# Kernel tuning notes

Hardware: AMD Instinct MI355X
Metric: run time of the kernel (lower is better)

The kernel has to match this reference:

```python
import jax, jax.numpy as jnp
import numpy as np

H = 1024
B_DIM = 64  # bottleneck
EPS = 1e-5

def setup_inputs() -> dict:
    key = jax.random.key(0)
    ks = jax.random.split(key, 5)
    x = jax.random.normal(ks[0], (8, 4096, H), dtype=jnp.float32)
    norm_w = jnp.ones((H,), jnp.float32)
    norm_b = jnp.zeros((H,), jnp.float32)
    # nn.Linear default init ~ U(-1/sqrt(fan_in), 1/sqrt(fan_in))
    lim_d = 1.0 / np.sqrt(H)
    down_w = jax.random.uniform(ks[1], (B_DIM, H), jnp.float32, -lim_d, lim_d)
    down_b = jax.random.uniform(ks[2], (B_DIM,), jnp.float32, -lim_d, lim_d)
    # NOTE: original inits up to zeros; we use small random values so the
    # computation (and gradients) are non-degenerate for kernel testing.
    lim_u = 1.0 / np.sqrt(B_DIM)
    up_w = jax.random.uniform(ks[3], (H, B_DIM), jnp.float32, -lim_u, lim_u)
    up_b = jax.random.uniform(ks[4], (H,), jnp.float32, -lim_u, lim_u)
    return {"x": x, "norm_w": norm_w, "norm_b": norm_b,
            "down_w": down_w, "down_b": down_b, "up_w": up_w, "up_b": up_b}

def reference(x, norm_w, norm_b, down_w, down_b, up_w, up_b):
    # LayerNorm over last dim, eps=1e-5 (PyTorch default)
    mu = jnp.mean(x, axis=-1, keepdims=True)
    var = jnp.mean(jnp.square(x - mu), axis=-1, keepdims=True)
    xn = (x - mu) * jax.lax.rsqrt(var + EPS) * norm_w + norm_b
    # down-proj [B,S,H] @ [H,b] -> [B,S,b]
    h = jnp.einsum('bsh,dh->bsd', xn, down_w) + down_b
    h = jax.nn.gelu(h, approximate=False)  # torch nn.GELU default = exact erf
    # up-proj [B,S,b] @ [b,H] -> [B,S,H], residual add
    out = jnp.einsum('bsd,hd->bsh', h, up_w) + up_b
    return x + out
```

## Files before the change

kernel.cpp:

```cpp
#include <hip/hip_runtime.h>


#define HDIM 1024
#define BDIM 64
#define RT   32
#define XPAD 1032
#define GPAD 72

using s16x8 = __attribute__((ext_vector_type(8))) short;
using s16x4 = __attribute__((ext_vector_type(4))) short;
using f32x4 = __attribute__((ext_vector_type(4))) float;
using f32x2 = __attribute__((ext_vector_type(2))) float;

__device__ __forceinline__ short f2bf(float f) {
  unsigned u = __builtin_bit_cast(unsigned, f);
  u += 0x7fffu + ((u >> 16) & 1u);
  return (short)(u >> 16);
}
__device__ __forceinline__ float bf2f(short s) {
  unsigned u = ((unsigned)(unsigned short)s) << 16;
  return __builtin_bit_cast(float, u);
}

extern "C" __global__ void prep_weights(const float* __restrict__ dw,
                                        const float* __restrict__ uw,
                                        short* __restrict__ wsbf) {
  int tid = blockIdx.x * 256 + threadIdx.x;
  const float* src = (tid < 8192) ? dw : uw;
  int off = (tid < 8192) ? tid * 8 : (tid - 8192) * 8;
  f32x4 v0 = *(const f32x4*)(src + off);
  f32x4 v1 = *(const f32x4*)(src + off + 4);
  s16x8 o;
#pragma unroll
  for (int k = 0; k < 4; ++k) { o[k] = f2bf(v0[k]); o[k + 4] = f2bf(v1[k]); }
  *(s16x8*)(wsbf + tid * 8) = o;
}

extern "C" __global__ __launch_bounds__(512, 4)
void adapter_fused(const float* __restrict__ x,
                   const float* __restrict__ nw, const float* __restrict__ nb,
                   const float* __restrict__ db, const float* __restrict__ ub,
                   const short* __restrict__ dwb, const short* __restrict__ uwb,
                   float* __restrict__ out)
{
  __shared__ __align__(16) short xnbf[RT][XPAD];
  __shared__ __align__(16) short gbf[RT][GPAD];
  __shared__ float wln[HDIM];
  __shared__ float bln[HDIM];

  const int t  = threadIdx.x;
  const int rb = blockIdx.x * RT;

  {
    f32x2 w2 = ((const f32x2*)nw)[t];
    f32x2 b2 = ((const f32x2*)nb)[t];
    *(f32x2*)&wln[t * 2] = w2;
    *(f32x2*)&bln[t * 2] = b2;
  }

  const int r  = t >> 4;
  const int cl = t & 15;
  const float* xrow = x + (size_t)(rb + r) * HDIM;
  float sum = 0.f, ssq = 0.f;
#pragma unroll 8
  for (int i = 0; i < 16; ++i) {
    int j4 = i * 16 + cl;
    f32x4 v = ((const f32x4*)xrow)[j4];
    s16x4 s;
#pragma unroll
    for (int k = 0; k < 4; ++k) { float f = v[k]; sum += f; ssq += f * f; s[k] = f2bf(f); }
    *(s16x4*)&xnbf[r][j4 * 4] = s;
  }
#pragma unroll
  for (int m = 1; m < 16; m <<= 1) {
    sum += __shfl_xor(sum, m);
    ssq += __shfl_xor(ssq, m);
  }
  const float mu  = sum * (1.0f / HDIM);
  const float var = ssq * (1.0f / HDIM) - mu * mu;
  const float rs  = rsqrtf(var + 1e-5f);

#pragma unroll
  for (int i = 0; i < 16; ++i) {
    int j = (i * 16 + cl) * 4;
    s16x4 s = *(const s16x4*)&xnbf[r][j];
    s16x4 o;
#pragma unroll
    for (int k = 0; k < 4; ++k) {
      float xf = bf2f(s[k]);
      o[k] = f2bf((xf - mu) * rs * wln[j + k] + bln[j + k]);
    }
    *(s16x4*)&xnbf[r][j] = o;
  }
  __syncthreads();

  const int w    = t >> 6;
  const int lane = t & 63;
  const int q    = lane >> 4;
  const int c    = lane & 15;
  const int rt   = w & 1;
  const int ct   = w >> 1;
  f32x4 acc = {0.f, 0.f, 0.f, 0.f};
  const short* dwrow = dwb + (size_t)(ct * 16 + c) * HDIM;
#pragma unroll 4
  for (int ks = 0; ks < 32; ++ks) {
    int k0 = ks * 32 + q * 8;
    s16x8 a = *(const s16x8*)&xnbf[rt * 16 + c][k0];
    s16x8 b = *(const s16x8*)(dwrow + k0);
    acc = __builtin_amdgcn_mfma_f32_16x16x32_bf16(a, b, acc, 0, 0, 0);
  }

  {
    float dbv = db[ct * 16 + c];
#pragma unroll
    for (int i = 0; i < 4; ++i) {
      float hv = acc[i] + dbv;
      float g  = 0.5f * hv * (1.0f + erff(hv * 0.70710678118654752f));
      gbf[rt * 16 + q * 4 + i][ct * 16 + c] = f2bf(g);
    }
  }
  __syncthreads();

  s16x8 a0 = *(const s16x8*)&gbf[rt * 16 + c][q * 8];
  s16x8 a1 = *(const s16x8*)&gbf[rt * 16 + c][32 + q * 8];
  const float* xbase = x   + (size_t)(rb + rt * 16) * HDIM;
  float*       obase = out + (size_t)(rb + rt * 16) * HDIM;
#pragma unroll 2
  for (int nt = 0; nt < 16; ++nt) {
    int ncol = ct * 256 + nt * 16 + c;
    const short* uwrow = uwb + (size_t)ncol * BDIM;
    s16x8 b0 = *(const s16x8*)(uwrow + q * 8);
    s16x8 b1 = *(const s16x8*)(uwrow + 32 + q * 8);
    f32x4 o4 = {0.f, 0.f, 0.f, 0.f};
    o4 = __builtin_amdgcn_mfma_f32_16x16x32_bf16(a0, b0, o4, 0, 0, 0);
    o4 = __builtin_amdgcn_mfma_f32_16x16x32_bf16(a1, b1, o4, 0, 0, 0);
    float ubv = ub[ncol];
#pragma unroll
    for (int i = 0; i < 4; ++i) {
      int ro = (q * 4 + i) * HDIM + ncol;
      obase[ro] = o4[i] + ubv + xbase[ro];
    }
  }
}

extern "C" void kernel_launch(void* const* d_in, const int* in_sizes, int n_in,
                              void* d_out, int out_size, void* d_ws, size_t ws_size,
                              hipStream_t stream) {
  const float* x  = (const float*)d_in[0];
  const float* nw = (const float*)d_in[1];
  const float* nb = (const float*)d_in[2];
  const float* dw = (const float*)d_in[3];
  const float* db = (const float*)d_in[4];
  const float* uw = (const float*)d_in[5];
  const float* ub = (const float*)d_in[6];
  float* out = (float*)d_out;

  short* wsbf = (short*)d_ws;
  prep_weights<<<64, 256, 0, stream>>>(dw, uw, wsbf);

  const int rows = in_sizes[0] / HDIM;
  const int grid = rows / RT;
  adapter_fused<<<grid, 512, 0, stream>>>(x, nw, nb, db, ub,
                                          wsbf, wsbf + 65536, out);
}
```

Baseline: 290.1 us.

## Make adapter kernel persistent over row tiles with register-resident weights and double buffering

Each 1024-thread block now walks 8 tiles of 16 rows. The bf16 down and up projection weights are held in registers for the whole block instead of being re-read from global memory per tile. The next tile's x rows are loaded while the current tile runs its MFMAs, and the normalized rows go into a double-buffered LDS array. The down-projection K dimension is split across 4 wave groups and reduced through shared memory. The trade-off is extra barriers and LDS partial-sum traffic per tile, higher register pressure, and fewer blocks (256) to spread over the CUs.

Result: slower. 359.3 us (+23.8%).

```diff
diff --git a/kernel.cpp b/kernel.cpp
--- a/kernel.cpp
+++ b/kernel.cpp
@@ -3,23 +3,19 @@
 
 #define HDIM 1024
 #define BDIM 64
-#define RT   32
+#define RT   16
+#define NT   8
 #define XPAD 1032
 #define GPAD 72
 
 using s16x8 = __attribute__((ext_vector_type(8))) short;
 using s16x4 = __attribute__((ext_vector_type(4))) short;
 using f32x4 = __attribute__((ext_vector_type(4))) float;
-using f32x2 = __attribute__((ext_vector_type(2))) float;
 
 __device__ __forceinline__ short f2bf(float f) {
   unsigned u = __builtin_bit_cast(unsigned, f);
   u += 0x7fffu + ((u >> 16) & 1u);
   return (short)(u >> 16);
-}
-__device__ __forceinline__ float bf2f(short s) {
-  unsigned u = ((unsigned)(unsigned short)s) << 16;
-  return __builtin_bit_cast(float, u);
 }
 
 extern "C" __global__ void prep_weights(const float* __restrict__ dw,
@@ -36,110 +32,131 @@
   *(s16x8*)(wsbf + tid * 8) = o;
 }
 
-extern "C" __global__ __launch_bounds__(512, 4)
+extern "C" __global__ __launch_bounds__(1024, 4)
 void adapter_fused(const float* __restrict__ x,
                    const float* __restrict__ nw, const float* __restrict__ nb,
                    const float* __restrict__ db, const float* __restrict__ ub,
                    const short* __restrict__ dwb, const short* __restrict__ uwb,
                    float* __restrict__ out)
 {
-  __shared__ __align__(16) short xnbf[RT][XPAD];
+  __shared__ __align__(16) short xn[2][RT][XPAD];
+  __shared__ float part[4][4][16][16];
   __shared__ __align__(16) short gbf[RT][GPAD];
   __shared__ float wln[HDIM];
   __shared__ float bln[HDIM];
 
-  const int t  = threadIdx.x;
-  const int rb = blockIdx.x * RT;
-
-  {
-    f32x2 w2 = ((const f32x2*)nw)[t];
-    f32x2 b2 = ((const f32x2*)nb)[t];
-    *(f32x2*)&wln[t * 2] = w2;
-    *(f32x2*)&bln[t * 2] = b2;
-  }
-
-  const int r  = t >> 4;
-  const int cl = t & 15;
-  const float* xrow = x + (size_t)(rb + r) * HDIM;
-  float sum = 0.f, ssq = 0.f;
-#pragma unroll 8
-  for (int i = 0; i < 16; ++i) {
-    int j4 = i * 16 + cl;
-    f32x4 v = ((const f32x4*)xrow)[j4];
-    s16x4 s;
-#pragma unroll
-    for (int k = 0; k < 4; ++k) { float f = v[k]; sum += f; ssq += f * f; s[k] = f2bf(f); }
-    *(s16x4*)&xnbf[r][j4 * 4] = s;
-  }
-#pragma unroll
-  for (int m = 1; m < 16; m <<= 1) {
-    sum += __shfl_xor(sum, m);
-    ssq += __shfl_xor(ssq, m);
-  }
-  const float mu  = sum * (1.0f / HDIM);
-  const float var = ssq * (1.0f / HDIM) - mu * mu;
-  const float rs  = rsqrtf(var + 1e-5f);
-
-#pragma unroll
-  for (int i = 0; i < 16; ++i) {
-    int j = (i * 16 + cl) * 4;
-    s16x4 s = *(const s16x4*)&xnbf[r][j];
-    s16x4 o;
-#pragma unroll
-    for (int k = 0; k < 4; ++k) {
-      float xf = bf2f(s[k]);
-      o[k] = f2bf((xf - mu) * rs * wln[j + k] + bln[j + k]);
-    }
-    *(s16x4*)&xnbf[r][j] = o;
-  }
-  __syncthreads();
-
+  const int t    = threadIdx.x;
   const int w    = t >> 6;
   const int lane = t & 63;
   const int q    = lane >> 4;
   const int c    = lane & 15;
-  const int rt   = w & 1;
-  const int ct   = w >> 1;
-  f32x4 acc = {0.f, 0.f, 0.f, 0.f};
-  const short* dwrow = dwb + (size_t)(ct * 16 + c) * HDIM;
-#pragma unroll 4
-  for (int ks = 0; ks < 32; ++ks) {
-    int k0 = ks * 32 + q * 8;
-    s16x8 a = *(const s16x8*)&xnbf[rt * 16 + c][k0];
-    s16x8 b = *(const s16x8*)(dwrow + k0);
-    acc = __builtin_amdgcn_mfma_f32_16x16x32_bf16(a, b, acc, 0, 0, 0);
+  const int ct   = w & 3;
+  const int kt   = w >> 2;
+
+  wln[t] = nw[t];
+  bln[t] = nb[t];
+
+  s16x8 bdw[8];
+  {
+    const short* p = dwb + (size_t)(ct * 16 + c) * HDIM + kt * 256 + q * 8;
+#pragma unroll
+    for (int s = 0; s < 8; ++s) bdw[s] = *(const s16x8*)(p + s * 32);
   }
+  s16x8 buw[4][2];
+  float ubr[4];
+#pragma unroll
+  for (int j = 0; j < 4; ++j) {
+    const short* p = uwb + (size_t)(w * 64 + j * 16 + c) * BDIM + q * 8;
+    buw[j][0] = *(const s16x8*)(p);
+    buw[j][1] = *(const s16x8*)(p + 32);
+    ubr[j] = ub[w * 64 + j * 16 + c];
+  }
+  const float dbr = db[ct * 16 + c];
 
-  {
-    float dbv = db[ct * 16 + c];
+  const size_t rowbase = (size_t)blockIdx.x * (RT * NT);
+
+  f32x4 xv[4];
+  auto load_tile = [&](int tile) {
+    const f32x4* xr = (const f32x4*)(x + (rowbase + tile * RT + w) * HDIM);
+#pragma unroll
+    for (int i = 0; i < 4; ++i) xv[i] = xr[i * 64 + lane];
+  };
+  auto stats_store = [&](int buf) {
+    float sum = 0.f, ssq = 0.f;
+#pragma unroll
+    for (int i = 0; i < 4; ++i)
+#pragma unroll
+      for (int k = 0; k < 4; ++k) { float f = xv[i][k]; sum += f; ssq += f * f; }
+#pragma unroll
+    for (int m = 1; m < 64; m <<= 1) {
+      sum += __shfl_xor(sum, m);
+      ssq += __shfl_xor(ssq, m);
+    }
+    const float mu  = sum * (1.0f / HDIM);
+    const float var = ssq * (1.0f / HDIM) - mu * mu;
+    const float rs  = rsqrtf(var + 1e-5f);
 #pragma unroll
     for (int i = 0; i < 4; ++i) {
-      float hv = acc[i] + dbv;
-      float g  = 0.5f * hv * (1.0f + erff(hv * 0.70710678118654752f));
-      gbf[rt * 16 + q * 4 + i][ct * 16 + c] = f2bf(g);
+      int j = (i * 64 + lane) * 4;
+      f32x4 lw = *(const f32x4*)&wln[j];
+      f32x4 lb = *(const f32x4*)&bln[j];
+      s16x4 o;
+#pragma unroll
+      for (int k = 0; k < 4; ++k)
+        o[k] = f2bf((xv[i][k] - mu) * rs * lw[k] + lb[k]);
+      *(s16x4*)&xn[buf][w][j] = o;
     }
-  }
+  };
+
+  load_tile(0);
+  __syncthreads();
+  stats_store(0);
   __syncthreads();
 
-  s16x8 a0 = *(const s16x8*)&gbf[rt * 16 + c][q * 8];
-  s16x8 a1 = *(const s16x8*)&gbf[rt * 16 + c][32 + q * 8];
-  const float* xbase = x   + (size_t)(rb + rt * 16) * HDIM;
-  float*       obase = out + (size_t)(rb + rt * 16) * HDIM;
-#pragma unroll 2
-  for (int nt = 0; nt < 16; ++nt) {
-    int ncol = ct * 256 + nt * 16 + c;
-    const short* uwrow = uwb + (size_t)ncol * BDIM;
-    s16x8 b0 = *(const s16x8*)(uwrow + q * 8);
-    s16x8 b1 = *(const s16x8*)(uwrow + 32 + q * 8);
-    f32x4 o4 = {0.f, 0.f, 0.f, 0.f};
-    o4 = __builtin_amdgcn_mfma_f32_16x16x32_bf16(a0, b0, o4, 0, 0, 0);
-    o4 = __builtin_amdgcn_mfma_f32_16x16x32_bf16(a1, b1, o4, 0, 0, 0);
-    float ubv = ub[ncol];
+  for (int tile = 0; tile < NT; ++tile) {
+    const int cur = tile & 1, nxt = cur ^ 1;
+    load_tile(tile + 1 < NT ? tile + 1 : tile);
+
+    f32x4 acc = {0.f, 0.f, 0.f, 0.f};
 #pragma unroll
-    for (int i = 0; i < 4; ++i) {
-      int ro = (q * 4 + i) * HDIM + ncol;
-      obase[ro] = o4[i] + ubv + xbase[ro];
+    for (int s = 0; s < 8; ++s) {
+      s16x8 a = *(const s16x8*)&xn[cur][c][kt * 256 + s * 32 + q * 8];
+      acc = __builtin_amdgcn_mfma_f32_16x16x32_bf16(a, bdw[s], acc, 0, 0, 0);
     }
+#pragma unroll
+    for (int i = 0; i < 4; ++i)
+      part[kt][ct][q * 4 + i][c] = acc[i];
+    __syncthreads();
+
+    {
+      const int rq = w >> 2;
+      const int m  = rq * 4 + q;
+      float h = part[0][ct][m][c] + part[1][ct][m][c]
+              + part[2][ct][m][c] + part[3][ct][m][c] + dbr;
+      float g = 0.5f * h * (1.0f + erff(h * 0.70710678118654752f));
+      gbf[m][ct * 16 + c] = f2bf(g);
+    }
+    __syncthreads();
+
+    s16x8 a0 = *(const s16x8*)&gbf[c][q * 8];
+    s16x8 a1 = *(const s16x8*)&gbf[c][32 + q * 8];
+    const float* xres = x   + (rowbase + tile * RT) * HDIM;
+    float*       ob   = out + (rowbase + tile * RT) * HDIM;
+#pragma unroll
+    for (int j = 0; j < 4; ++j) {
+      f32x4 o4 = {0.f, 0.f, 0.f, 0.f};
+      o4 = __builtin_amdgcn_mfma_f32_16x16x32_bf16(a0, buw[j][0], o4, 0, 0, 0);
+      o4 = __builtin_amdgcn_mfma_f32_16x16x32_bf16(a1, buw[j][1], o4, 0, 0, 0);
+      const int col = w * 64 + j * 16 + c;
+#pragma unroll
+      for (int i = 0; i < 4; ++i) {
+        int ro = (q * 4 + i) * HDIM + col;
+        ob[ro] = o4[i] + ubr[j] + xres[ro];
+      }
+    }
+
+    stats_store(nxt);
+    __syncthreads();
   }
 }
 
@@ -159,7 +176,7 @@
   prep_weights<<<64, 256, 0, stream>>>(dw, uw, wsbf);
 
   const int rows = in_sizes[0] / HDIM;
-  const int grid = rows / RT;
-  adapter_fused<<<grid, 512, 0, stream>>>(x, nw, nb, db, ub,
-                                          wsbf, wsbf + 65536, out);
+  const int grid = rows / (RT * NT);
+  adapter_fused<<<grid, 1024, 0, stream>>>(x, nw, nb, db, ub,
+                                           wsbf, wsbf + 65536, out);
 }
```
